# Kernel tuning notes

Hardware: AMD Instinct MI355X
Metric: run time of the kernel (lower is better)

## Reference

```python
import jax, jax.numpy as jnp
import numpy as np

B, N = 32, 4096
SA1 = (512, 0.2, 32)   # npoint, radius, nsample
SA2 = (128, 0.4, 64)
MLP1 = [3, 64, 64, 128]
MLP2 = [131, 128, 128, 256]   # 128 feats + 3 relative xyz
MLP3 = [259, 256, 512, 1024]  # 256 feats + 3 xyz (group_all)


def _mk_mlp(key, dims, prefix, d):
    for i in range(len(dims) - 1):
        key, k1 = jax.random.split(key)
        d[f"{prefix}_w{i}"] = jax.random.normal(k1, (dims[i], dims[i + 1]), jnp.float32) * (1.0 / np.sqrt(dims[i]))
        d[f"{prefix}_b{i}"] = jnp.zeros((dims[i + 1],), jnp.float32)
    return key


def setup_inputs() -> dict:
    key = jax.random.key(0)
    d = {}
    key, kx = jax.random.split(key)
    d["xyz"] = jax.random.uniform(kx, (B, N, 3), jnp.float32)  # normalized coords in [0,1)
    key = _mk_mlp(key, MLP1, "sa1", d)
    key = _mk_mlp(key, MLP2, "sa2", d)
    key = _mk_mlp(key, MLP3, "sa3", d)
    key, k1, k2 = jax.random.split(key, 3)
    d["cls_w"] = jax.random.normal(k1, (1024, 1), jnp.float32) * 0.03
    d["cls_b"] = jnp.zeros((1,), jnp.float32)
    d["reg_w"] = jax.random.normal(k2, (1024, 4), jnp.float32) * 0.03
    d["reg_b"] = jnp.zeros((4,), jnp.float32)
    return d


def fps(xyz, npoint):
    """Farthest point sampling. xyz: (B,N,3) -> idx (B,npoint) int32."""
    Bb, Nn, _ = xyz.shape

    def step(carry, _):
        dist, farthest = carry  # (B,N), (B,)
        centroid = jnp.take_along_axis(xyz, farthest[:, None, None], axis=1)  # (B,1,3)
        d = jnp.sum((xyz - centroid) ** 2, axis=-1)  # (B,N)
        dist = jnp.minimum(dist, d)
        nxt = jnp.argmax(dist, axis=-1).astype(jnp.int32)
        return (dist, nxt), farthest

    init = (jnp.full((Bb, Nn), 1e10, xyz.dtype), jnp.zeros((Bb,), jnp.int32))
    _, idx = jax.lax.scan(step, init, None, length=npoint)
    return idx.T  # (B,npoint)


def ball_query(radius, nsample, xyz, new_xyz):
    """xyz: (B,N,3), new_xyz: (B,S,3) -> idx (B,S,nsample) int32."""
    Bb, S, _ = new_xyz.shape
    Nn = xyz.shape[1]
    sqr = jnp.sum((new_xyz[:, :, None, :] - xyz[:, None, :, :]) ** 2, axis=-1)  # (B,S,N)
    idx = jnp.broadcast_to(jnp.arange(Nn, dtype=jnp.int32), (Bb, S, Nn))
    idx = jnp.where(sqr > radius * radius, Nn, idx)
    idx = jnp.sort(idx, axis=-1)[:, :, :nsample]
    first = idx[:, :, :1]
    return jnp.where(idx == Nn, first, idx)  # pad out-of-ball slots with first neighbor


def _sa(xyz, feats, npoint, radius, nsample, ws, bs):
    Bb = xyz.shape[0]
    cidx = fps(xyz, npoint)
    new_xyz = xyz[jnp.arange(Bb)[:, None], cidx]  # (B,S,3)
    gidx = ball_query(radius, nsample, xyz, new_xyz)  # (B,S,K)
    b3 = jnp.arange(Bb)[:, None, None]
    g = xyz[b3, gidx] - new_xyz[:, :, None, :]  # (B,S,K,3) relative coords
    if feats is not None:
        g = jnp.concatenate([g, feats[b3, gidx]], axis=-1)
    for w, b in zip(ws, bs):
        g = jax.nn.relu(g @ w + b)
    return new_xyz, jnp.max(g, axis=2)  # (B,S,C_out)


def _sa_all(xyz, feats, ws, bs):
    g = jnp.concatenate([xyz, feats], axis=-1)[:, None]  # (B,1,S,3+C)
    for w, b in zip(ws, bs):
        g = jax.nn.relu(g @ w + b)
    return jnp.max(g, axis=2)[:, 0]  # (B,C_out)


def reference(xyz, sa1_w0, sa1_b0, sa1_w1, sa1_b1, sa1_w2, sa1_b2,
              sa2_w0, sa2_b0, sa2_w1, sa2_b1, sa2_w2, sa2_b2,
              sa3_w0, sa3_b0, sa3_w1, sa3_b1, sa3_w2, sa3_b2,
              cls_w, cls_b, reg_w, reg_b):
    xyz1, f1 = _sa(xyz, None, SA1[0], SA1[1], SA1[2],
                   [sa1_w0, sa1_w1, sa1_w2], [sa1_b0, sa1_b1, sa1_b2])
    xyz2, f2 = _sa(xyz1, f1, SA2[0], SA2[1], SA2[2],
                   [sa2_w0, sa2_w1, sa2_w2], [sa2_b0, sa2_b1, sa2_b2])
    feat = _sa_all(xyz2, f2, [sa3_w0, sa3_w1, sa3_w2], [sa3_b0, sa3_b1, sa3_b2])  # (B,1024)
    return feat @ cls_w + cls_b, feat @ reg_w + reg_b
```

## Files before the change

kernel.cpp:

```cpp
#include <hip/hip_runtime.h>
#include <hip/hip_bf16.h>

#define DEVINL __device__ __forceinline__

typedef __attribute__((ext_vector_type(8))) short bf16x8;
typedef __attribute__((ext_vector_type(8))) unsigned short u16x8;
typedef __attribute__((ext_vector_type(4))) float f32x4;

DEVINL unsigned short f2bh(float f){
  __hip_bfloat16 h = __float2bfloat16(f);
  return __bfloat16_as_ushort(h);
}
DEVINL float bh2f(unsigned short h){ return __uint_as_float(((unsigned)h) << 16); }

DEVINL unsigned long long dpp_max_u64(unsigned long long k) {
#define DPP_STEP(ctrl)                                                        \
  {                                                                           \
    int hi = (int)(k >> 32), lo = (int)(unsigned)k;                           \
    int oh = __builtin_amdgcn_update_dpp(0, hi, ctrl, 0xF, 0xF, 1);           \
    int ol = __builtin_amdgcn_update_dpp(0, lo, ctrl, 0xF, 0xF, 1);           \
    unsigned long long ok =                                                   \
        ((unsigned long long)(unsigned)oh << 32) | (unsigned)ol;              \
    if (ok > k) k = ok;                                                       \
  }
  DPP_STEP(0x111)
  DPP_STEP(0x112)
  DPP_STEP(0x114)
  DPP_STEP(0x118)
  DPP_STEP(0x142)
  DPP_STEP(0x143)
#undef DPP_STEP
  return k;
}

template<int N, int NP, int NT>
DEVINL void fps_body(const float* __restrict__ xyz, float* __restrict__ nxyz,
                     int b, int t) {
  constexpr int PTS = N / NT;
  constexpr int NW = NT / 64;
  __shared__ float xs[N], ys[N], zs[N];
  __shared__ int farr[NP];
  __shared__ unsigned long long sk[2][(NW > 1 ? NW : 1)];
  float px[PTS], py[PTS], pz[PTS], dst[PTS];
  const float* base = xyz + (size_t)b * N * 3;
#pragma unroll
  for (int j = 0; j < PTS; ++j) {
    int i = t + j * NT;
    float x = base[i * 3 + 0], y = base[i * 3 + 1], z = base[i * 3 + 2];
    px[j] = x; py[j] = y; pz[j] = z;
    xs[i] = x; ys[i] = y; zs[i] = z;
    dst[j] = 1e10f;
  }
  if constexpr (NW > 1) __syncthreads();
  int far = 0;
  const int wv = t >> 6, ln = t & 63;
  for (int s = 0; s < NP; ++s) {
    float cx = xs[far], cy = ys[far], cz = zs[far];
    if (t == 0) farr[s] = far;
    float bv = -1.f; int bi = 0;
#pragma unroll
    for (int j = 0; j < PTS; ++j) {
      float dx = __fsub_rn(px[j], cx), dy = __fsub_rn(py[j], cy), dz = __fsub_rn(pz[j], cz);
      float d = __fadd_rn(__fadd_rn(__fmul_rn(dx, dx), __fmul_rn(dy, dy)), __fmul_rn(dz, dz));
      float nd = fminf(dst[j], d);
      dst[j] = nd;
      int i = t + j * NT;
      if (nd > bv) { bv = nd; bi = i; }
    }
    unsigned long long key =
        ((unsigned long long)__float_as_uint(bv) << 32) | (unsigned)(~bi);
    key = dpp_max_u64(key);
    if constexpr (NW == 1) {
      int rl = __builtin_amdgcn_readlane((int)(unsigned)key, 63);
      far = (int)(~(unsigned)rl);
    } else {
      const int p = s & 1;
      if (ln == 63) sk[p][wv] = key;
      __syncthreads();
      unsigned long long m = sk[p][0];
#pragma unroll
      for (int q = 1; q < NW; ++q) {
        unsigned long long qk = sk[p][q];
        if (qk > m) m = qk;
      }
      far = (int)(~(unsigned)m);
    }
  }
  if constexpr (NW > 1) __syncthreads();
  for (int s2 = t; s2 < NP; s2 += NT) {
    int fi = farr[s2];
    float* o = nxyz + ((size_t)b * NP + s2) * 3;
    o[0] = xs[fi]; o[1] = ys[fi]; o[2] = zs[fi];
  }
}

template<int N, int NS>
DEVINL void bq_body(const float* __restrict__ pts, const float* __restrict__ centers,
                    int* __restrict__ gidx, int Q, float r2, int blk, int t) {
  const int wv = t >> 6, ln = t & 63;
  const int g = blk * 4 + wv;
  const int b = g / Q, q = g % Q;
  const float* pb = pts + (size_t)b * N * 3;
  const float* c = centers + ((size_t)b * Q + q) * 3;
  const float cx = c[0], cy = c[1], cz = c[2];
  __shared__ int gbuf[4][NS];
  float nx = pb[ln * 3 + 0], ny = pb[ln * 3 + 1], nz = pb[ln * 3 + 2];
  int taken = 0;
  for (int base = 0; base < N; base += 64) {
    const float x = nx, y = ny, z = nz;
    if (base + 64 < N) {
      const float* np = pb + (size_t)(base + 64 + ln) * 3;
      nx = np[0]; ny = np[1]; nz = np[2];
    }
    int i = base + ln;
    float dx = __fsub_rn(x, cx), dy = __fsub_rn(y, cy), dz = __fsub_rn(z, cz);
    float d = __fadd_rn(__fadd_rn(__fmul_rn(dx, dx), __fmul_rn(dy, dy)), __fmul_rn(dz, dz));
    bool in = (d <= r2);
    unsigned long long mk = __ballot(in);
    int rank = __popcll(mk & ((1ull << ln) - 1ull));
    int pos = taken + rank;
    if (in && pos < NS) gbuf[wv][pos] = i;
    taken += (int)__popcll(mk);
    if (taken >= NS) break;
  }
  int total = taken < NS ? taken : NS;
  int first = gbuf[wv][0];
  int* out = gidx + ((size_t)b * Q + q) * NS;
  for (int j = ln; j < NS; j += 64) out[j] = (j < total) ? gbuf[wv][j] : first;
}

struct WPEnt { const float* W; unsigned short* hi; unsigned short* lo; int K, N, row0, beg, end; };
struct WPTab { WPEnt e[8]; };
DEVINL void wprep_body(const WPTab& tab, int idx) {
#pragma unroll
  for (int i = 0; i < 8; ++i) {
    const WPEnt& E = tab.e[i];
    if (idx >= E.beg && idx < E.end) {
      int local = idx - E.beg;
      int k = local / E.N, n = local - k * E.N;
      float v = E.W[(size_t)(E.row0 + k) * E.N + n];
      unsigned short h = f2bh(v);
      E.hi[(size_t)n * E.K + k] = h;
      E.lo[(size_t)n * E.K + k] = f2bh(v - bh2f(h));
    }
  }
}

__global__ __launch_bounds__(256) void fps1_wprep_kernel(const float* __restrict__ xyz,
                                                         float* __restrict__ nx1, WPTab tab) {
  if (blockIdx.x < 32) { fps_body<4096, 512, 256>(xyz, nx1, blockIdx.x, threadIdx.x); return; }
  wprep_body(tab, (blockIdx.x - 32) * 256 + threadIdx.x);
}

__global__ __launch_bounds__(256) void fps2_bq1_kernel(const float* __restrict__ xyz,
                                                       const float* __restrict__ nx1,
                                                       int* __restrict__ gidx1,
                                                       float* __restrict__ nx2, float r21) {
  if (blockIdx.x < 32) {
    if (threadIdx.x < 64) fps_body<512, 128, 64>(nx1, nx2, blockIdx.x, threadIdx.x);
    return;
  }
  bq_body<4096, 32>(xyz, nx1, gidx1, 512, r21, blockIdx.x - 32, threadIdx.x);
}

template<int K, int N, int CW, int AS, int WS, int NTH>
DEVINL void do_layer(const unsigned short* __restrict__ Ghi, const unsigned short* __restrict__ Glo,
                     const float* __restrict__ A, unsigned short* __restrict__ Whi,
                     unsigned short* __restrict__ Wlo, f32x4* acc, int t) {
  constexpr int KT = K / 32;
  constexpr int NCH = N / CW;
  constexpr int K8 = K / 8;
  constexpr int SI = (CW * K8) / NTH;
  constexpr int CT = CW / 16;
  const int l = t & 63, wv = t >> 6;

  u16x8 rh[SI], rl[SI];
#pragma unroll
  for (int s = 0; s < SI; ++s) {
    int u = t + s * NTH;
    int nn = u / K8, k8 = (u - nn * K8) * 8;
    rh[s] = *reinterpret_cast<const u16x8*>(Ghi + (size_t)nn * K + k8);
    rl[s] = *reinterpret_cast<const u16x8*>(Glo + (size_t)nn * K + k8);
  }

  bf16x8 ahi[KT], alo[KT];
  {
    const int row = wv * 16 + (l & 15);
    const float* ap = A + row * AS + (l >> 4) * 8;
#pragma unroll
    for (int kt = 0; kt < KT; ++kt) {
      float4 v0 = *reinterpret_cast<const float4*>(ap + kt * 32);
      float4 v1 = *reinterpret_cast<const float4*>(ap + kt * 32 + 4);
      float f[8] = {v0.x, v0.y, v0.z, v0.w, v1.x, v1.y, v1.z, v1.w};
      bf16x8 h, lo2;
#pragma unroll
      for (int j = 0; j < 8; ++j) {
        unsigned short hb = f2bh(f[j]);
        h[j] = (short)hb;
        lo2[j] = (short)f2bh(f[j] - bh2f(hb));
      }
      ahi[kt] = h; alo[kt] = lo2;
    }
  }
#pragma unroll
  for (int i = 0; i < N / 16; ++i) acc[i] = f32x4{0.f, 0.f, 0.f, 0.f};

#pragma unroll
  for (int c = 0; c < NCH; ++c) {
    __syncthreads();
#pragma unroll
    for (int s = 0; s < SI; ++s) {
      int u = t + s * NTH;
      int nn = u / K8, k8 = (u - nn * K8) * 8;
      *reinterpret_cast<u16x8*>(Whi + nn * WS + k8) = rh[s];
      *reinterpret_cast<u16x8*>(Wlo + nn * WS + k8) = rl[s];
    }
    if (c + 1 < NCH) {
#pragma unroll
      for (int s = 0; s < SI; ++s) {
        int u = t + s * NTH;
        int nn = u / K8, k8 = (u - nn * K8) * 8;
        rh[s] = *reinterpret_cast<const u16x8*>(Ghi + (size_t)((c + 1) * CW + nn) * K + k8);
        rl[s] = *reinterpret_cast<const u16x8*>(Glo + (size_t)((c + 1) * CW + nn) * K + k8);
      }
    }
    __syncthreads();
#pragma unroll
    for (int ct = 0; ct < CT; ++ct) {
      const unsigned short* wp = Whi + (ct * 16 + (l & 15)) * WS + (l >> 4) * 8;
      const unsigned short* wq = Wlo + (ct * 16 + (l & 15)) * WS + (l >> 4) * 8;
      f32x4 a = acc[c * CT + ct];
#pragma unroll
      for (int kt = 0; kt < KT; ++kt) {
        bf16x8 wh = *reinterpret_cast<const bf16x8*>(wp + kt * 32);
        bf16x8 wl = *reinterpret_cast<const bf16x8*>(wq + kt * 32);
        a = __builtin_amdgcn_mfma_f32_16x16x32_bf16(ahi[kt], wh, a, 0, 0, 0);
        a = __builtin_amdgcn_mfma_f32_16x16x32_bf16(alo[kt], wh, a, 0, 0, 0);
        a = __builtin_amdgcn_mfma_f32_16x16x32_bf16(ahi[kt], wl, a, 0, 0, 0);
      }
      acc[c * CT + ct] = a;
    }
  }
}

template<int K, int N, int CW, int WS, int NTH>
DEVINL void do_layer0_gather(const unsigned short* __restrict__ Ghi,
                             const unsigned short* __restrict__ Glo,
                             const float* __restrict__ Wxyz,
                             const unsigned short* __restrict__ f1h,
                             const unsigned short* __restrict__ f1l,
                             const int* __restrict__ idxs, const float* __restrict__ sxyz,
                             unsigned short* __restrict__ Whi, unsigned short* __restrict__ Wlo,
                             f32x4* acc, int t) {
  constexpr int KT = K / 32;
  constexpr int NCH = N / CW;
  constexpr int K8 = K / 8;
  constexpr int SI = (CW * K8) / NTH;
  constexpr int CT = CW / 16;
  const int l = t & 63, wv = t >> 6;

  u16x8 rh[SI], rl[SI];
#pragma unroll
  for (int s = 0; s < SI; ++s) {
    int u = t + s * NTH;
    int nn = u / K8, k8 = (u - nn * K8) * 8;
    rh[s] = *reinterpret_cast<const u16x8*>(Ghi + (size_t)nn * K + k8);
    rl[s] = *reinterpret_cast<const u16x8*>(Glo + (size_t)nn * K + k8);
  }

  bf16x8 ahi[KT], alo[KT];
  {
    const int row = wv * 16 + (l & 15);
    const int i = idxs[row];
    const unsigned short* hp = f1h + (size_t)i * K + (l >> 4) * 8;
    const unsigned short* lp = f1l + (size_t)i * K + (l >> 4) * 8;
#pragma unroll
    for (int kt = 0; kt < KT; ++kt) {
      ahi[kt] = *reinterpret_cast<const bf16x8*>(hp + kt * 32);
      alo[kt] = *reinterpret_cast<const bf16x8*>(lp + kt * 32);
    }
  }
#pragma unroll
  for (int i = 0; i < N / 16; ++i) acc[i] = f32x4{0.f, 0.f, 0.f, 0.f};

#pragma unroll
  for (int c = 0; c < NCH; ++c) {
    __syncthreads();
#pragma unroll
    for (int s = 0; s < SI; ++s) {
      int u = t + s * NTH;
      int nn = u / K8, k8 = (u - nn * K8) * 8;
      *reinterpret_cast<u16x8*>(Whi + nn * WS + k8) = rh[s];
      *reinterpret_cast<u16x8*>(Wlo + nn * WS + k8) = rl[s];
    }
    if (c + 1 < NCH) {
#pragma unroll
      for (int s = 0; s < SI; ++s) {
        int u = t + s * NTH;
        int nn = u / K8, k8 = (u - nn * K8) * 8;
        rh[s] = *reinterpret_cast<const u16x8*>(Ghi + (size_t)((c + 1) * CW + nn) * K + k8);
        rl[s] = *reinterpret_cast<const u16x8*>(Glo + (size_t)((c + 1) * CW + nn) * K + k8);
      }
    }
    __syncthreads();
#pragma unroll
    for (int ct = 0; ct < CT; ++ct) {
      const unsigned short* wp = Whi + (ct * 16 + (l & 15)) * WS + (l >> 4) * 8;
      const unsigned short* wq = Wlo + (ct * 16 + (l & 15)) * WS + (l >> 4) * 8;
      f32x4 a = acc[c * CT + ct];
#pragma unroll
      for (int kt = 0; kt < KT; ++kt) {
        bf16x8 wh = *reinterpret_cast<const bf16x8*>(wp + kt * 32);
        bf16x8 wl = *reinterpret_cast<const bf16x8*>(wq + kt * 32);
        a = __builtin_amdgcn_mfma_f32_16x16x32_bf16(ahi[kt], wh, a, 0, 0, 0);
        a = __builtin_amdgcn_mfma_f32_16x16x32_bf16(alo[kt], wh, a, 0, 0, 0);
        a = __builtin_amdgcn_mfma_f32_16x16x32_bf16(ahi[kt], wl, a, 0, 0, 0);
      }
      acc[c * CT + ct] = a;
    }
  }
  {
    float xr[4][3];
#pragma unroll
    for (int r = 0; r < 4; ++r) {
      int row = wv * 16 + (l >> 4) * 4 + r;
      xr[r][0] = sxyz[row * 4 + 0];
      xr[r][1] = sxyz[row * 4 + 1];
      xr[r][2] = sxyz[row * 4 + 2];
    }
#pragma unroll
    for (int gt = 0; gt < N / 16; ++gt) {
      int col = gt * 16 + (l & 15);
      float w0 = Wxyz[col], w1 = Wxyz[N + col], w2 = Wxyz[2 * N + col];
#pragma unroll
      for (int r = 0; r < 4; ++r)
        acc[gt][r] += xr[r][0] * w0 + xr[r][1] * w1 + xr[r][2] * w2;
    }
  }
}

template<int NPTS, int Q, int M, int GPB, int FD, int C1, int C2, int C3>
__global__ __launch_bounds__(512) void sa2_kernel(
    const float* __restrict__ pts, const float* __restrict__ centers,
    const int* __restrict__ gidx,
    const unsigned short* __restrict__ f1h, const unsigned short* __restrict__ f1l,
    const float* __restrict__ W0, const float* __restrict__ B0,
    const unsigned short* __restrict__ G0h, const unsigned short* __restrict__ G0l,
    const unsigned short* __restrict__ G1h, const unsigned short* __restrict__ G1l,
    const float* __restrict__ B1,
    const unsigned short* __restrict__ G2h, const unsigned short* __restrict__ G2l,
    const float* __restrict__ B2,
    float* __restrict__ fout) {
  constexpr int NTH = 512;
  constexpr int ROWS = M * GPB;
  constexpr int NWV = NTH / 64;
  static_assert(ROWS == 16 * NWV, "wave owns 16 rows");
  constexpr int MAXK = (C1 > C2 ? C1 : C2);
  constexpr int AS = MAXK + 12;
  constexpr int WS = MAXK + 8;
  constexpr int CW = 128;
  __shared__ __align__(16) float A[ROWS * AS];
  __shared__ __align__(16) unsigned short Whi[CW * WS];
  __shared__ __align__(16) unsigned short Wlo[CW * WS];
  __shared__ float sxyz[ROWS * 4];
  __shared__ int idxs[ROWS];
  __shared__ float ctr[GPB][4];
  __shared__ float red[NWV][C3];

  const int t = threadIdx.x;
  const int blk = blockIdx.x;
  const int b = blk / (Q / GPB);
  const int q0 = (blk % (Q / GPB)) * GPB;
  const int l = t & 63, wv = t >> 6;

  if (t < GPB * 3) {
    int g = t / 3, c2 = t % 3;
    ctr[g][c2] = centers[((size_t)b * Q + q0 + g) * 3 + c2];
  }
  for (int m = t; m < ROWS; m += NTH)
    idxs[m] = gidx[((size_t)b * Q + q0 + (m / M)) * M + (m % M)];
  __syncthreads();
  const float* pb = pts + (size_t)b * NPTS * 3;
  for (int u = t; u < ROWS * 3; u += NTH) {
    int m = u / 3, cmp = u - m * 3;
    int g = m / M, i = idxs[m];
    sxyz[m * 4 + cmp] = pb[i * 3 + cmp] - ctr[g][cmp];
  }
  __syncthreads();

  f32x4 acc[C3 / 16];

  do_layer0_gather<FD, C1, CW, WS, NTH>(
      G0h, G0l, W0, f1h + (size_t)b * NPTS * FD, f1l + (size_t)b * NPTS * FD,
      idxs, sxyz, Whi, Wlo, acc, t);
#pragma unroll
  for (int gt = 0; gt < C1 / 16; ++gt) {
    int col = gt * 16 + (l & 15);
    float bia = B0[col];
#pragma unroll
    for (int r = 0; r < 4; ++r)
      A[(wv * 16 + (l >> 4) * 4 + r) * AS + col] = fmaxf(acc[gt][r] + bia, 0.f);
  }

  do_layer<C1, C2, CW, AS, WS, NTH>(G1h, G1l, A, Whi, Wlo, acc, t);
#pragma unroll
  for (int gt = 0; gt < C2 / 16; ++gt) {
    int col = gt * 16 + (l & 15);
    float bia = B1[col];
#pragma unroll
    for (int r = 0; r < 4; ++r)
      A[(wv * 16 + (l >> 4) * 4 + r) * AS + col] = fmaxf(acc[gt][r] + bia, 0.f);
  }

  do_layer<C2, C3, CW, AS, WS, NTH>(G2h, G2l, A, Whi, Wlo, acc, t);
#pragma unroll
  for (int gt = 0; gt < C3 / 16; ++gt) {
    int col = gt * 16 + (l & 15);
    float v = fmaxf(fmaxf(acc[gt][0], acc[gt][1]), fmaxf(acc[gt][2], acc[gt][3]));
    v = fmaxf(v, __shfl_xor(v, 16, 64));
    v = fmaxf(v, __shfl_xor(v, 32, 64));
    if (l < 16) red[wv][col] = v + B2[col];
  }
  __syncthreads();
  constexpr int WPG = NWV / GPB;
  for (int u = t; u < GPB * C3; u += NTH) {
    int g = u / C3, c2 = u - g * C3;
    float v = red[g * WPG][c2];
#pragma unroll
    for (int w = 1; w < WPG; ++w) v = fmaxf(v, red[g * WPG + w][c2]);
    fout[((size_t)b * Q + q0 + g) * C3 + c2] = fmaxf(v, 0.f);
  }
}

template<int NPTS, int Q, int M, int GPB, int TPB>
DEVINL void sa1_body(const float* __restrict__ pts, const float* __restrict__ centers,
                     const int* __restrict__ gidx,
                     const float* __restrict__ W0, const float* __restrict__ B0,
                     const unsigned short* __restrict__ G1h, const unsigned short* __restrict__ G1l,
                     const float* __restrict__ B1,
                     const unsigned short* __restrict__ G2h, const unsigned short* __restrict__ G2l,
                     const float* __restrict__ B2,
                     unsigned short* __restrict__ f1h, unsigned short* __restrict__ f1l,
                     int sblk, int t) {
  static_assert(M * GPB == 64, "");
  constexpr int C1 = 64, C2 = 64, C3 = 128;
  constexpr int AS = 76;
  constexpr int WS = 72;
  constexpr int NC = C2 + C3;
  __shared__ __align__(16) float A[64 * AS];
  __shared__ __align__(16) unsigned short Wh[NC * WS];
  __shared__ __align__(16) unsigned short Wl[NC * WS];
  __shared__ float sxyz[64 * 4];
  __shared__ int idxs[64];
  __shared__ float ctr[GPB][4];
  __shared__ float red[4][C3];

  const int l = t & 63, wv = t >> 6;

  for (int u = t; u < NC * 8; u += 256) {
    int col = u >> 3, k8 = (u & 7) * 8;
    const unsigned short* sh = (col < C2) ? G1h + (size_t)col * 64 + k8
                                          : G2h + (size_t)(col - C2) * 64 + k8;
    const unsigned short* sl = (col < C2) ? G1l + (size_t)col * 64 + k8
                                          : G2l + (size_t)(col - C2) * 64 + k8;
    *reinterpret_cast<u16x8*>(Wh + col * WS + k8) = *reinterpret_cast<const u16x8*>(sh);
    *reinterpret_cast<u16x8*>(Wl + col * WS + k8) = *reinterpret_cast<const u16x8*>(sl);
  }

  for (int it = 0; it < TPB; ++it) {
    const int blk = sblk * TPB + it;
    const int b = blk / (Q / GPB);
    const int q0 = (blk % (Q / GPB)) * GPB;

    if (t < GPB * 3) {
      int g = t / 3, c2 = t % 3;
      ctr[g][c2] = centers[((size_t)b * Q + q0 + g) * 3 + c2];
    }
    for (int m = t; m < 64; m += 256)
      idxs[m] = gidx[((size_t)b * Q + q0 + (m / M)) * M + (m % M)];
    __syncthreads();
    const float* pb = pts + (size_t)b * NPTS * 3;
    for (int u = t; u < 64 * 3; u += 256) {
      int m = u / 3, cmp = u - m * 3;
      int g = m / M, i = idxs[m];
      sxyz[m * 4 + cmp] = pb[i * 3 + cmp] - ctr[g][cmp];
    }
    __syncthreads();

    for (int u = t; u < 64 * C1; u += 256) {
      int m = u / C1, c2 = u - m * C1;
      float v = B0[c2] + sxyz[m * 4 + 0] * W0[0 * C1 + c2]
                       + sxyz[m * 4 + 1] * W0[1 * C1 + c2]
                       + sxyz[m * 4 + 2] * W0[2 * C1 + c2];
      A[m * AS + c2] = fmaxf(v, 0.f);
    }
    __syncthreads();

    f32x4 acc[8];
    {
      bf16x8 ah[2], al[2];
      const float* ap = A + (wv * 16 + (l & 15)) * AS + (l >> 4) * 8;
#pragma unroll
      for (int kt = 0; kt < 2; ++kt) {
        float4 v0 = *reinterpret_cast<const float4*>(ap + kt * 32);
        float4 v1 = *reinterpret_cast<const float4*>(ap + kt * 32 + 4);
        float f[8] = {v0.x, v0.y, v0.z, v0.w, v1.x, v1.y, v1.z, v1.w};
        bf16x8 h, lo2;
#pragma unroll
        for (int j = 0; j < 8; ++j) {
          unsigned short hb = f2bh(f[j]);
          h[j] = (short)hb;
          lo2[j] = (short)f2bh(f[j] - bh2f(hb));
        }
        ah[kt] = h; al[kt] = lo2;
      }
#pragma unroll
      for (int i = 0; i < 4; ++i) acc[i] = f32x4{0.f, 0.f, 0.f, 0.f};
#pragma unroll
      for (int ct = 0; ct < 4; ++ct) {
        const unsigned short* wp = Wh + (ct * 16 + (l & 15)) * WS + (l >> 4) * 8;
        const unsigned short* wq = Wl + (ct * 16 + (l & 15)) * WS + (l >> 4) * 8;
        f32x4 a = acc[ct];
#pragma unroll
        for (int kt = 0; kt < 2; ++kt) {
          bf16x8 wh = *reinterpret_cast<const bf16x8*>(wp + kt * 32);
          bf16x8 wl = *reinterpret_cast<const bf16x8*>(wq + kt * 32);
          a = __builtin_amdgcn_mfma_f32_16x16x32_bf16(ah[kt], wh, a, 0, 0, 0);
          a = __builtin_amdgcn_mfma_f32_16x16x32_bf16(al[kt], wh, a, 0, 0, 0);
          a = __builtin_amdgcn_mfma_f32_16x16x32_bf16(ah[kt], wl, a, 0, 0, 0);
        }
        acc[ct] = a;
      }
#pragma unroll
      for (int gt = 0; gt < 4; ++gt) {
        int col = gt * 16 + (l & 15);
        float bia = B1[col];
#pragma unroll
        for (int r = 0; r < 4; ++r)
          A[(wv * 16 + (l >> 4) * 4 + r) * AS + col] = fmaxf(acc[gt][r] + bia, 0.f);
      }
    }

    {
      bf16x8 ah[2], al[2];
      const float* ap = A + (wv * 16 + (l & 15)) * AS + (l >> 4) * 8;
#pragma unroll
      for (int kt = 0; kt < 2; ++kt) {
        float4 v0 = *reinterpret_cast<const float4*>(ap + kt * 32);
        float4 v1 = *reinterpret_cast<const float4*>(ap + kt * 32 + 4);
        float f[8] = {v0.x, v0.y, v0.z, v0.w, v1.x, v1.y, v1.z, v1.w};
        bf16x8 h, lo2;
#pragma unroll
        for (int j = 0; j < 8; ++j) {
          unsigned short hb = f2bh(f[j]);
          h[j] = (short)hb;
          lo2[j] = (short)f2bh(f[j] - bh2f(hb));
        }
        ah[kt] = h; al[kt] = lo2;
      }
#pragma unroll
      for (int i = 0; i < 8; ++i) acc[i] = f32x4{0.f, 0.f, 0.f, 0.f};
#pragma unroll
      for (int gt = 0; gt < 8; ++gt) {
        const unsigned short* wp = Wh + (C2 + gt * 16 + (l & 15)) * WS + (l >> 4) * 8;
        const unsigned short* wq = Wl + (C2 + gt * 16 + (l & 15)) * WS + (l >> 4) * 8;
        f32x4 a = acc[gt];
#pragma unroll
        for (int kt = 0; kt < 2; ++kt) {
          bf16x8 wh = *reinterpret_cast<const bf16x8*>(wp + kt * 32);
          bf16x8 wl = *reinterpret_cast<const bf16x8*>(wq + kt * 32);
          a = __builtin_amdgcn_mfma_f32_16x16x32_bf16(ah[kt], wh, a, 0, 0, 0);
          a = __builtin_amdgcn_mfma_f32_16x16x32_bf16(al[kt], wh, a, 0, 0, 0);
          a = __builtin_amdgcn_mfma_f32_16x16x32_bf16(ah[kt], wl, a, 0, 0, 0);
        }
        acc[gt] = a;
      }
#pragma unroll
      for (int gt = 0; gt < 8; ++gt) {
        int col = gt * 16 + (l & 15);
        float v = fmaxf(fmaxf(acc[gt][0], acc[gt][1]), fmaxf(acc[gt][2], acc[gt][3]));
        v = fmaxf(v, __shfl_xor(v, 16, 64));
        v = fmaxf(v, __shfl_xor(v, 32, 64));
        if (l < 16) red[wv][col] = v + B2[col];
      }
    }
    __syncthreads();
    constexpr int WPG = 4 / GPB;
    for (int u = t; u < GPB * C3; u += 256) {
      int g = u / C3, c2 = u - g * C3;
      float v = red[g * WPG][c2];
#pragma unroll
      for (int w = 1; w < WPG; ++w) v = fmaxf(v, red[g * WPG + w][c2]);
      v = fmaxf(v, 0.f);
      size_t o = ((size_t)b * Q + q0 + g) * C3 + c2;
      unsigned short h = f2bh(v);
      f1h[o] = h;
      f1l[o] = f2bh(v - bh2f(h));
    }
    __syncthreads();
  }
}

__global__ __launch_bounds__(256) void bq2_sa1_kernel(
    const float* __restrict__ xyz, const float* __restrict__ nx1,
    const float* __restrict__ nx2, int* __restrict__ gidx2, float r22,
    const int* __restrict__ gidx1,
    const float* __restrict__ s1w0, const float* __restrict__ s1b0,
    const unsigned short* __restrict__ g11h, const unsigned short* __restrict__ g11l,
    const float* __restrict__ s1b1,
    const unsigned short* __restrict__ g12h, const unsigned short* __restrict__ g12l,
    const float* __restrict__ s1b2,
    unsigned short* __restrict__ f1h, unsigned short* __restrict__ f1l) {
  if (blockIdx.x < 1024) {
    bq_body<512, 64>(nx1, nx2, gidx2, 128, r22, blockIdx.x, threadIdx.x);
    return;
  }
  sa1_body<4096, 512, 32, 2, 8>(xyz, nx1, gidx1, s1w0, s1b0, g11h, g11l, s1b1,
                                g12h, g12l, s1b2, f1h, f1l,
                                blockIdx.x - 1024, threadIdx.x);
}

constexpr int AS3 = 532;
DEVINL void sa3_frags(const float* __restrict__ A, int l, int KT, bf16x8* ahi, bf16x8* alo) {
  const float* ap = A + (l & 15) * AS3 + (l >> 4) * 8;
  for (int kt = 0; kt < KT; ++kt) {
    float4 v0 = *reinterpret_cast<const float4*>(ap + kt * 32);
    float4 v1 = *reinterpret_cast<const float4*>(ap + kt * 32 + 4);
    float f[8] = {v0.x, v0.y, v0.z, v0.w, v1.x, v1.y, v1.z, v1.w};
    bf16x8 h, lo2;
#pragma unroll
    for (int j = 0; j < 8; ++j) {
      unsigned short hb = f2bh(f[j]);
      h[j] = (short)hb;
      lo2[j] = (short)f2bh(f[j] - bh2f(hb));
    }
    ahi[kt] = h; alo[kt] = lo2;
  }
}

template<int CT, int K>
DEVINL void sa3_mmN(const unsigned short* __restrict__ Gh, const unsigned short* __restrict__ Gl,
                    int ncol0, int l, const bf16x8* ahi, const bf16x8* alo, f32x4* acc4) {
  constexpr int KT = K / 32;
#pragma unroll
  for (int ct = 0; ct < CT; ++ct) {
    const unsigned short* hp = Gh + (size_t)(ncol0 + ct * 16 + (l & 15)) * K + (l >> 4) * 8;
    const unsigned short* lp = Gl + (size_t)(ncol0 + ct * 16 + (l & 15)) * K + (l >> 4) * 8;
    f32x4 a = acc4[ct];
#pragma unroll
    for (int kt = 0; kt < KT; ++kt) {
      bf16x8 wh = *reinterpret_cast<const bf16x8*>(hp + kt * 32);
      bf16x8 wl = *reinterpret_cast<const bf16x8*>(lp + kt * 32);
      a = __builtin_amdgcn_mfma_f32_16x16x32_bf16(ahi[kt], wh, a, 0, 0, 0);
      a = __builtin_amdgcn_mfma_f32_16x16x32_bf16(alo[kt], wh, a, 0, 0, 0);
      a = __builtin_amdgcn_mfma_f32_16x16x32_bf16(ahi[kt], wl, a, 0, 0, 0);
    }
    acc4[ct] = a;
  }
}

__global__ __launch_bounds__(512) void sa3f_kernel(
    const float* __restrict__ nx2, const float* __restrict__ f2,
    const float* __restrict__ W0full,
    const unsigned short* __restrict__ G0h, const unsigned short* __restrict__ G0l,
    const float* __restrict__ B0,
    const unsigned short* __restrict__ G1h, const unsigned short* __restrict__ G1l,
    const float* __restrict__ B1,
    const unsigned short* __restrict__ G2h, const unsigned short* __restrict__ G2l,
    const float* __restrict__ B2,
    float* __restrict__ partial) {
  __shared__ __align__(16) float A[16 * AS3];
  __shared__ float sxyz[16][4];
  const int t = threadIdx.x, l = t & 63, w = t >> 6;
  const int b = blockIdx.x >> 3, rb = blockIdx.x & 7;
  const int row0 = rb * 16;
  {
    int r = t >> 5, cc = (t & 31) * 8;
    const float* src = f2 + ((size_t)b * 128 + row0 + r) * 256 + cc;
    float* dstp = A + r * AS3 + cc;
#pragma unroll
    for (int j = 0; j < 8; j += 4)
      *reinterpret_cast<float4*>(dstp + j) = *reinterpret_cast<const float4*>(src + j);
    if (t < 16) {
      const float* s = nx2 + ((size_t)b * 128 + row0 + t) * 3;
      sxyz[t][0] = s[0]; sxyz[t][1] = s[1]; sxyz[t][2] = s[2];
    }
  }
  __syncthreads();

  {
    bf16x8 ah[8], al[8];
    sa3_frags(A, l, 8, ah, al);
    __syncthreads();
    f32x4 acc[2];
#pragma unroll
    for (int i = 0; i < 2; ++i) acc[i] = f32x4{0.f, 0.f, 0.f, 0.f};
    sa3_mmN<2, 256>(G0h, G0l, w * 32, l, ah, al, acc);
    float xr[4][3];
#pragma unroll
    for (int r = 0; r < 4; ++r) {
      int row = (l >> 4) * 4 + r;
      xr[r][0] = sxyz[row][0]; xr[r][1] = sxyz[row][1]; xr[r][2] = sxyz[row][2];
    }
#pragma unroll
    for (int ct = 0; ct < 2; ++ct) {
      int col = w * 32 + ct * 16 + (l & 15);
      float w0 = W0full[col], w1 = W0full[256 + col], w2 = W0full[512 + col];
      float bia = B0[col];
#pragma unroll
      for (int r = 0; r < 4; ++r) {
        int row = (l >> 4) * 4 + r;
        float v = acc[ct][r] + xr[r][0] * w0 + xr[r][1] * w1 + xr[r][2] * w2 + bia;
        A[row * AS3 + col] = fmaxf(v, 0.f);
      }
    }
    __syncthreads();
  }

  {
    bf16x8 ah[8], al[8];
    sa3_frags(A, l, 8, ah, al);
    __syncthreads();
    f32x4 acc[4];
#pragma unroll
    for (int i = 0; i < 4; ++i) acc[i] = f32x4{0.f, 0.f, 0.f, 0.f};
    sa3_mmN<4, 256>(G1h, G1l, w * 64, l, ah, al, acc);
#pragma unroll
    for (int cc = 0; cc < 4; ++cc) {
      int col = w * 64 + cc * 16 + (l & 15);
      float bia = B1[col];
#pragma unroll
      for (int r = 0; r < 4; ++r) {
        int row = (l >> 4) * 4 + r;
        A[row * AS3 + col] = fmaxf(acc[cc][r] + bia, 0.f);
      }
    }
    __syncthreads();
  }

  {
    bf16x8 ah[16], al[16];
    sa3_frags(A, l, 16, ah, al);
    float* pout = partial + ((size_t)(b * 8 + rb)) * 1024;
#pragma unroll
    for (int sub = 0; sub < 2; ++sub) {
      f32x4 acc[4];
#pragma unroll
      for (int i = 0; i < 4; ++i) acc[i] = f32x4{0.f, 0.f, 0.f, 0.f};
      sa3_mmN<4, 512>(G2h, G2l, w * 128 + sub * 64, l, ah, al, acc);
#pragma unroll
      for (int ct = 0; ct < 4; ++ct) {
        int col = w * 128 + sub * 64 + ct * 16 + (l & 15);
        float v = fmaxf(fmaxf(acc[ct][0], acc[ct][1]), fmaxf(acc[ct][2], acc[ct][3]));
        v = fmaxf(v, __shfl_xor(v, 16, 64));
        v = fmaxf(v, __shfl_xor(v, 32, 64));
        if (l < 16) pout[col] = v + B2[col];
      }
    }
  }
}

__global__ __launch_bounds__(256) void heads_kernel(const float* __restrict__ partial,
                                                    const float* __restrict__ cw,
                                                    const float* __restrict__ cb,
                                                    const float* __restrict__ rw,
                                                    const float* __restrict__ rb,
                                                    float* __restrict__ out) {
  const int b = blockIdx.x, t = threadIdx.x;
  const float* pb = partial + (size_t)b * 8 * 1024;
  float a0 = 0, a1 = 0, a2 = 0, a3 = 0, a4 = 0;
  for (int k = t; k < 1024; k += 256) {
    float m = pb[k];
#pragma unroll
    for (int p = 1; p < 8; ++p) m = fmaxf(m, pb[p * 1024 + k]);
    float f = fmaxf(m, 0.f);
    a0 += f * cw[k];
    const float* r = rw + (size_t)k * 4;
    a1 += f * r[0]; a2 += f * r[1]; a3 += f * r[2]; a4 += f * r[3];
  }
#pragma unroll
  for (int m = 32; m >= 1; m >>= 1) {
    a0 += __shfl_xor(a0, m, 64); a1 += __shfl_xor(a1, m, 64);
    a2 += __shfl_xor(a2, m, 64); a3 += __shfl_xor(a3, m, 64);
    a4 += __shfl_xor(a4, m, 64);
  }
  __shared__ float red[4][5];
  const int wv = t >> 6, ln = t & 63;
  if (ln == 0) { red[wv][0] = a0; red[wv][1] = a1; red[wv][2] = a2; red[wv][3] = a3; red[wv][4] = a4; }
  __syncthreads();
  if (t == 0) {
    float s0 = red[0][0] + red[1][0] + red[2][0] + red[3][0];
    float s1 = red[0][1] + red[1][1] + red[2][1] + red[3][1];
    float s2 = red[0][2] + red[1][2] + red[2][2] + red[3][2];
    float s3 = red[0][3] + red[1][3] + red[2][3] + red[3][3];
    float s4 = red[0][4] + red[1][4] + red[2][4] + red[3][4];
    out[b] = s0 + cb[0];
    out[32 + b * 4 + 0] = s1 + rb[0];
    out[32 + b * 4 + 1] = s2 + rb[1];
    out[32 + b * 4 + 2] = s3 + rb[2];
    out[32 + b * 4 + 3] = s4 + rb[3];
  }
}

extern "C" void kernel_launch(void* const* d_in, const int* in_sizes, int n_in,
                              void* d_out, int out_size, void* d_ws, size_t ws_size,
                              hipStream_t stream) {
  (void)in_sizes; (void)n_in; (void)out_size; (void)ws_size;
  const float* xyz  = (const float*)d_in[0];
  const float* s1w0 = (const float*)d_in[1];  const float* s1b0 = (const float*)d_in[2];
  const float* s1w1 = (const float*)d_in[3];  const float* s1b1 = (const float*)d_in[4];
  const float* s1w2 = (const float*)d_in[5];  const float* s1b2 = (const float*)d_in[6];
  const float* s2w0 = (const float*)d_in[7];  const float* s2b0 = (const float*)d_in[8];
  const float* s2w1 = (const float*)d_in[9];  const float* s2b1 = (const float*)d_in[10];
  const float* s2w2 = (const float*)d_in[11]; const float* s2b2 = (const float*)d_in[12];
  const float* s3w0 = (const float*)d_in[13]; const float* s3b0 = (const float*)d_in[14];
  const float* s3w1 = (const float*)d_in[15]; const float* s3b1 = (const float*)d_in[16];
  const float* s3w2 = (const float*)d_in[17]; const float* s3b2 = (const float*)d_in[18];
  const float* clsw = (const float*)d_in[19]; const float* clsb = (const float*)d_in[20];
  const float* regw = (const float*)d_in[21]; const float* regb = (const float*)d_in[22];

  char* ws = (char*)d_ws;
  float* nx1   = (float*)(ws + 0);
  int*   gidx1 = (int*)  (ws + 196608);
  unsigned short* f1h = (unsigned short*)(ws + 2293760);
  unsigned short* f1l = (unsigned short*)(ws + 6488064);
  float* nx2   = (float*)(ws + 10682368);
  int*   gidx2 = (int*)  (ws + 10731520);
  float* f2    = (float*)(ws + 11780096);

  unsigned short* wt = (unsigned short*)(ws + 20168704);
  unsigned short* g11h = wt;
  unsigned short* g11l = wt + 4096;
  unsigned short* g12h = wt + 8192;
  unsigned short* g12l = wt + 16384;
  unsigned short* g20h = wt + 24576;
  unsigned short* g20l = wt + 40960;
  unsigned short* g21h = wt + 57344;
  unsigned short* g21l = wt + 73728;
  unsigned short* g22h = wt + 90112;
  unsigned short* g22l = wt + 122880;
  unsigned short* g30h = (unsigned short*)(ws + 20480000);
  unsigned short* g30l = (unsigned short*)(ws + 20611072);
  unsigned short* g31h = (unsigned short*)(ws + 20742144);
  unsigned short* g31l = (unsigned short*)(ws + 21004288);
  unsigned short* g32h = (unsigned short*)(ws + 21266432);
  unsigned short* g32l = (unsigned short*)(ws + 22315008);
  float* partial = (float*)(ws + 23363584);

  const float r21 = (float)(0.2 * 0.2);
  const float r22 = (float)(0.4 * 0.4);

  WPTab tab;
  int off = 0;
  auto set = [&](int i, const float* W, unsigned short* hi, unsigned short* lo,
                 int K, int N, int row0) {
    tab.e[i] = WPEnt{W, hi, lo, K, N, row0, off, off + K * N};
    off += K * N;
  };
  set(0, s1w1, g11h, g11l, 64, 64, 0);
  set(1, s1w2, g12h, g12l, 64, 128, 0);
  set(2, s2w0, g20h, g20l, 128, 128, 3);
  set(3, s2w1, g21h, g21l, 128, 128, 0);
  set(4, s2w2, g22h, g22l, 128, 256, 0);
  set(5, s3w0, g30h, g30l, 256, 256, 3);
  set(6, s3w1, g31h, g31l, 256, 512, 0);
  set(7, s3w2, g32h, g32l, 512, 1024, 0);
  const int wblocks = (off + 255) / 256;

  fps1_wprep_kernel<<<32 + wblocks, 256, 0, stream>>>(xyz, nx1, tab);
  fps2_bq1_kernel<<<32 + 4096, 256, 0, stream>>>(xyz, nx1, gidx1, nx2, r21);
  bq2_sa1_kernel<<<1024 + 1024, 256, 0, stream>>>(
      xyz, nx1, nx2, gidx2, r22, gidx1,
      s1w0, s1b0, g11h, g11l, s1b1, g12h, g12l, s1b2, f1h, f1l);
  sa2_kernel<512, 128, 64, 2, 128, 128, 128, 256><<<2048, 512, 0, stream>>>(
      nx1, nx2, gidx2, f1h, f1l, s2w0, s2b0,
      g20h, g20l, g21h, g21l, s2b1, g22h, g22l, s2b2, f2);
  sa3f_kernel<<<256, 512, 0, stream>>>(nx2, f2, s3w0, g30h, g30l, s3b0,
                                       g31h, g31l, s3b1, g32h, g32l, s3b2, partial);
  heads_kernel<<<32, 256, 0, stream>>>(partial, clsw, clsb, regw, regb, (float*)d_out);
}
```

Measured before the change: 638.5 us.

## Fuse heads into sa3 via last-block atomic counter; drop shared index staging

The separate heads kernel is removed. Each sa3 block bumps a per-batch atomic counter after writing its partial max, and the last of the eight blocks does the final max-reduction and the cls/reg dot products, which saves a kernel launch. The counters are zeroed in the first kernel. The sa2/sa1 kernels also stop staging gather indices and centers in shared memory and read them straight from global, which removes a __syncthreads or two. In exchange there are redundant global index reads, and the fused heads path relies on threadfence ordering.

```diff
diff --git a/kernel.cpp b/kernel.cpp
--- a/kernel.cpp
+++ b/kernel.cpp
@@ -147,8 +147,10 @@
 }
 
 __global__ __launch_bounds__(256) void fps1_wprep_kernel(const float* __restrict__ xyz,
-                                                         float* __restrict__ nx1, WPTab tab) {
+                                                         float* __restrict__ nx1, WPTab tab,
+                                                         int* __restrict__ counters) {
   if (blockIdx.x < 32) { fps_body<4096, 512, 256>(xyz, nx1, blockIdx.x, threadIdx.x); return; }
+  if (blockIdx.x == 32 && threadIdx.x < 32) counters[threadIdx.x] = 0;
   wprep_body(tab, (blockIdx.x - 32) * 256 + threadIdx.x);
 }
 
@@ -243,13 +245,14 @@
   }
 }
 
-template<int K, int N, int CW, int WS, int NTH>
+template<int K, int N, int CW, int WS, int NTH, int M>
 DEVINL void do_layer0_gather(const unsigned short* __restrict__ Ghi,
                              const unsigned short* __restrict__ Glo,
                              const float* __restrict__ Wxyz,
                              const unsigned short* __restrict__ f1h,
                              const unsigned short* __restrict__ f1l,
-                             const int* __restrict__ idxs, const float* __restrict__ sxyz,
+                             const int* __restrict__ gidx_base,
+                             const float* __restrict__ sxyz,
                              unsigned short* __restrict__ Whi, unsigned short* __restrict__ Wlo,
                              f32x4* acc, int t) {
   constexpr int KT = K / 32;
@@ -271,7 +274,7 @@
   bf16x8 ahi[KT], alo[KT];
   {
     const int row = wv * 16 + (l & 15);
-    const int i = idxs[row];
+    const int i = gidx_base[(row / M) * M + (row % M)];
     const unsigned short* hp = f1h + (size_t)i * K + (l >> 4) * 8;
     const unsigned short* lp = f1l + (size_t)i * K + (l >> 4) * 8;
 #pragma unroll
@@ -363,8 +366,6 @@
   __shared__ __align__(16) unsigned short Whi[CW * WS];
   __shared__ __align__(16) unsigned short Wlo[CW * WS];
   __shared__ float sxyz[ROWS * 4];
-  __shared__ int idxs[ROWS];
-  __shared__ float ctr[GPB][4];
   __shared__ float red[NWV][C3];
 
   const int t = threadIdx.x;
@@ -373,26 +374,20 @@
   const int q0 = (blk % (Q / GPB)) * GPB;
   const int l = t & 63, wv = t >> 6;
 
-  if (t < GPB * 3) {
-    int g = t / 3, c2 = t % 3;
-    ctr[g][c2] = centers[((size_t)b * Q + q0 + g) * 3 + c2];
-  }
-  for (int m = t; m < ROWS; m += NTH)
-    idxs[m] = gidx[((size_t)b * Q + q0 + (m / M)) * M + (m % M)];
-  __syncthreads();
+  const int* gidx_base = gidx + ((size_t)b * Q + q0) * M;
   const float* pb = pts + (size_t)b * NPTS * 3;
   for (int u = t; u < ROWS * 3; u += NTH) {
     int m = u / 3, cmp = u - m * 3;
-    int g = m / M, i = idxs[m];
-    sxyz[m * 4 + cmp] = pb[i * 3 + cmp] - ctr[g][cmp];
-  }
-  __syncthreads();
+    int g = m / M;
+    int i = gidx_base[g * M + (m % M)];
+    sxyz[m * 4 + cmp] = pb[i * 3 + cmp] - centers[((size_t)b * Q + q0 + g) * 3 + cmp];
+  }
 
   f32x4 acc[C3 / 16];
 
-  do_layer0_gather<FD, C1, CW, WS, NTH>(
+  do_layer0_gather<FD, C1, CW, WS, NTH, M>(
       G0h, G0l, W0, f1h + (size_t)b * NPTS * FD, f1l + (size_t)b * NPTS * FD,
-      idxs, sxyz, Whi, Wlo, acc, t);
+      gidx_base, sxyz, Whi, Wlo, acc, t);
 #pragma unroll
   for (int gt = 0; gt < C1 / 16; ++gt) {
     int col = gt * 16 + (l & 15);
@@ -451,8 +446,6 @@
   __shared__ __align__(16) unsigned short Wh[NC * WS];
   __shared__ __align__(16) unsigned short Wl[NC * WS];
   __shared__ float sxyz[64 * 4];
-  __shared__ int idxs[64];
-  __shared__ float ctr[GPB][4];
   __shared__ float red[4][C3];
 
   const int l = t & 63, wv = t >> 6;
@@ -472,18 +465,13 @@
     const int b = blk / (Q / GPB);
     const int q0 = (blk % (Q / GPB)) * GPB;
 
-    if (t < GPB * 3) {
-      int g = t / 3, c2 = t % 3;
-      ctr[g][c2] = centers[((size_t)b * Q + q0 + g) * 3 + c2];
-    }
-    for (int m = t; m < 64; m += 256)
-      idxs[m] = gidx[((size_t)b * Q + q0 + (m / M)) * M + (m % M)];
-    __syncthreads();
+    const int* gidx_base = gidx + ((size_t)b * Q + q0) * M;
     const float* pb = pts + (size_t)b * NPTS * 3;
     for (int u = t; u < 64 * 3; u += 256) {
       int m = u / 3, cmp = u - m * 3;
-      int g = m / M, i = idxs[m];
-      sxyz[m * 4 + cmp] = pb[i * 3 + cmp] - ctr[g][cmp];
+      int g = m / M;
+      int i = gidx_base[g * M + (m % M)];
+      sxyz[m * 4 + cmp] = pb[i * 3 + cmp] - centers[((size_t)b * Q + q0 + g) * 3 + cmp];
     }
     __syncthreads();
 
@@ -668,12 +656,15 @@
     const float* __restrict__ B1,
     const unsigned short* __restrict__ G2h, const unsigned short* __restrict__ G2l,
     const float* __restrict__ B2,
-    float* __restrict__ partial) {
+    float* __restrict__ partial, int* __restrict__ counters,
+    const float* __restrict__ cw, const float* __restrict__ cb,
+    const float* __restrict__ rw, const float* __restrict__ rb,
+    float* __restrict__ out) {
   __shared__ __align__(16) float A[16 * AS3];
   __shared__ float sxyz[16][4];
   const int t = threadIdx.x, l = t & 63, w = t >> 6;
-  const int b = blockIdx.x >> 3, rb = blockIdx.x & 7;
-  const int row0 = rb * 16;
+  const int b = blockIdx.x >> 3, rb2 = blockIdx.x & 7;
+  const int row0 = rb2 * 16;
   {
     int r = t >> 5, cc = (t & 31) * 8;
     const float* src = f2 + ((size_t)b * 128 + row0 + r) * 256 + cc;
@@ -741,7 +732,7 @@
   {
     bf16x8 ah[16], al[16];
     sa3_frags(A, l, 16, ah, al);
-    float* pout = partial + ((size_t)(b * 8 + rb)) * 1024;
+    float* pout = partial + ((size_t)(b * 8 + rb2)) * 1024;
 #pragma unroll
     for (int sub = 0; sub < 2; ++sub) {
       f32x4 acc[4];
@@ -758,47 +749,48 @@
       }
     }
   }
-}
-
-__global__ __launch_bounds__(256) void heads_kernel(const float* __restrict__ partial,
-                                                    const float* __restrict__ cw,
-                                                    const float* __restrict__ cb,
-                                                    const float* __restrict__ rw,
-                                                    const float* __restrict__ rb,
-                                                    float* __restrict__ out) {
-  const int b = blockIdx.x, t = threadIdx.x;
-  const float* pb = partial + (size_t)b * 8 * 1024;
-  float a0 = 0, a1 = 0, a2 = 0, a3 = 0, a4 = 0;
-  for (int k = t; k < 1024; k += 256) {
-    float m = pb[k];
-#pragma unroll
-    for (int p = 1; p < 8; ++p) m = fmaxf(m, pb[p * 1024 + k]);
-    float f = fmaxf(m, 0.f);
-    a0 += f * cw[k];
-    const float* r = rw + (size_t)k * 4;
-    a1 += f * r[0]; a2 += f * r[1]; a3 += f * r[2]; a4 += f * r[3];
-  }
-#pragma unroll
-  for (int m = 32; m >= 1; m >>= 1) {
-    a0 += __shfl_xor(a0, m, 64); a1 += __shfl_xor(a1, m, 64);
-    a2 += __shfl_xor(a2, m, 64); a3 += __shfl_xor(a3, m, 64);
-    a4 += __shfl_xor(a4, m, 64);
-  }
-  __shared__ float red[4][5];
-  const int wv = t >> 6, ln = t & 63;
-  if (ln == 0) { red[wv][0] = a0; red[wv][1] = a1; red[wv][2] = a2; red[wv][3] = a3; red[wv][4] = a4; }
+
+  __threadfence();
   __syncthreads();
-  if (t == 0) {
-    float s0 = red[0][0] + red[1][0] + red[2][0] + red[3][0];
-    float s1 = red[0][1] + red[1][1] + red[2][1] + red[3][1];
-    float s2 = red[0][2] + red[1][2] + red[2][2] + red[3][2];
-    float s3 = red[0][3] + red[1][3] + red[2][3] + red[3][3];
-    float s4 = red[0][4] + red[1][4] + red[2][4] + red[3][4];
-    out[b] = s0 + cb[0];
-    out[32 + b * 4 + 0] = s1 + rb[0];
-    out[32 + b * 4 + 1] = s2 + rb[1];
-    out[32 + b * 4 + 2] = s3 + rb[2];
-    out[32 + b * 4 + 3] = s4 + rb[3];
+  __shared__ int slast;
+  if (t == 0) slast = atomicAdd(&counters[b], 1);
+  __syncthreads();
+  if (slast == 7) {
+    __threadfence();
+    const float* pb2 = partial + (size_t)b * 8 * 1024;
+    float a0 = 0, a1 = 0, a2 = 0, a3 = 0, a4 = 0;
+    if (t < 256) {
+      for (int k = t; k < 1024; k += 256) {
+        float m = pb2[k];
+#pragma unroll
+        for (int p = 1; p < 8; ++p) m = fmaxf(m, pb2[p * 1024 + k]);
+        float f = fmaxf(m, 0.f);
+        a0 += f * cw[k];
+        const float* r = rw + (size_t)k * 4;
+        a1 += f * r[0]; a2 += f * r[1]; a3 += f * r[2]; a4 += f * r[3];
+      }
+    }
+#pragma unroll
+    for (int m = 32; m >= 1; m >>= 1) {
+      a0 += __shfl_xor(a0, m, 64); a1 += __shfl_xor(a1, m, 64);
+      a2 += __shfl_xor(a2, m, 64); a3 += __shfl_xor(a3, m, 64);
+      a4 += __shfl_xor(a4, m, 64);
+    }
+    __shared__ float redh[8][5];
+    if (l == 0) { redh[w][0] = a0; redh[w][1] = a1; redh[w][2] = a2; redh[w][3] = a3; redh[w][4] = a4; }
+    __syncthreads();
+    if (t == 0) {
+      float s0 = redh[0][0] + redh[1][0] + redh[2][0] + redh[3][0];
+      float s1 = redh[0][1] + redh[1][1] + redh[2][1] + redh[3][1];
+      float s2 = redh[0][2] + redh[1][2] + redh[2][2] + redh[3][2];
+      float s3 = redh[0][3] + redh[1][3] + redh[2][3] + redh[3][3];
+      float s4 = redh[0][4] + redh[1][4] + redh[2][4] + redh[3][4];
+      out[b] = s0 + cb[0];
+      out[32 + b * 4 + 0] = s1 + rb[0];
+      out[32 + b * 4 + 1] = s2 + rb[1];
+      out[32 + b * 4 + 2] = s3 + rb[2];
+      out[32 + b * 4 + 3] = s4 + rb[3];
+    }
   }
 }
 
@@ -846,6 +838,7 @@
   unsigned short* g32h = (unsigned short*)(ws + 21266432);
   unsigned short* g32l = (unsigned short*)(ws + 22315008);
   float* partial = (float*)(ws + 23363584);
+  int* counters  = (int*)(ws + 24412160);
 
   const float r21 = (float)(0.2 * 0.2);
   const float r22 = (float)(0.4 * 0.4);
@@ -867,7 +860,7 @@
   set(7, s3w2, g32h, g32l, 512, 1024, 0);
   const int wblocks = (off + 255) / 256;
 
-  fps1_wprep_kernel<<<32 + wblocks, 256, 0, stream>>>(xyz, nx1, tab);
+  fps1_wprep_kernel<<<32 + wblocks, 256, 0, stream>>>(xyz, nx1, tab, counters);
   fps2_bq1_kernel<<<32 + 4096, 256, 0, stream>>>(xyz, nx1, gidx1, nx2, r21);
   bq2_sa1_kernel<<<1024 + 1024, 256, 0, stream>>>(
       xyz, nx1, nx2, gidx2, r22, gidx1,
@@ -876,6 +869,7 @@
       nx1, nx2, gidx2, f1h, f1l, s2w0, s2b0,
       g20h, g20l, g21h, g21l, s2b1, g22h, g22l, s2b2, f2);
   sa3f_kernel<<<256, 512, 0, stream>>>(nx2, f2, s3w0, g30h, g30l, s3b0,
-                                       g31h, g31l, s3b1, g32h, g32l, s3b2, partial);
-  heads_kernel<<<32, 256, 0, stream>>>(partial, clsw, clsb, regw, regb, (float*)d_out);
-}
+                                       g31h, g31l, s3b1, g32h, g32l, s3b2,
+                                       partial, counters, clsw, clsb, regw, regb,
+                                       (float*)d_out);
+}
```

After: 684.3 us. 7.2% more time.
